# Kernel tuning notes

Measured on AMD Instinct MI355X. Metric: run time of the kernel, lower is better.

The kernel has to match this reference:

```python
import jax, jax.numpy as jnp
import numpy as np

N_HEAD = 16
D_HEAD = 64
D_HIDN = 1024
B, S = 2, 2048
MASK_FILL = -1e9


def setup_inputs() -> dict:
    key = jax.random.key(0)
    ks = jax.random.split(key, 8)
    scale = 1.0 / np.sqrt(D_HIDN)
    return {
        "Q": jax.random.normal(ks[0], (B, S, D_HIDN), dtype=jnp.float32),
        "K": jax.random.normal(ks[1], (B, S, D_HIDN), dtype=jnp.float32),
        "V": jax.random.normal(ks[2], (B, S, D_HIDN), dtype=jnp.float32),
        "attn_mask": jnp.zeros((B, S, S), dtype=jnp.bool_),
        "Wq": jax.random.normal(ks[3], (D_HIDN, N_HEAD * D_HEAD), dtype=jnp.float32) * scale,
        "bq": jnp.zeros((N_HEAD * D_HEAD,), dtype=jnp.float32),
        "Wk": jax.random.normal(ks[4], (D_HIDN, N_HEAD * D_HEAD), dtype=jnp.float32) * scale,
        "bk": jnp.zeros((N_HEAD * D_HEAD,), dtype=jnp.float32),
        "Wv": jax.random.normal(ks[5], (D_HIDN, N_HEAD * D_HEAD), dtype=jnp.float32) * scale,
        "bv": jnp.zeros((N_HEAD * D_HEAD,), dtype=jnp.float32),
        "Wo": jax.random.normal(ks[6], (N_HEAD * D_HEAD, D_HIDN), dtype=jnp.float32) * scale,
        "bo": jnp.zeros((D_HIDN,), dtype=jnp.float32),
    }


def reference(Q, K, V, attn_mask, Wq, bq, Wk, bk, Wv, bv, Wo, bo):
    b, s, _ = Q.shape
    # projections -> [B, H, S, d_head]
    def split_heads(x):
        return x.reshape(b, -1, N_HEAD, D_HEAD).transpose(0, 2, 1, 3)
    q = split_heads(Q @ Wq + bq)
    k = split_heads(K @ Wk + bk)
    v = split_heads(V @ Wv + bv)
    # scaled dot-product attention with masked_fill(-1e9)
    scores = jnp.einsum("bhqd,bhkd->bhqk", q, k) / jnp.sqrt(jnp.float32(D_HEAD))
    scores = jnp.where(attn_mask[:, None, :, :], MASK_FILL, scores)
    attn_prob = jax.nn.softmax(scores, axis=-1)  # [B,H,S,S]
    context = jnp.einsum("bhqk,bhkd->bhqd", attn_prob, v)
    context = context.transpose(0, 2, 1, 3).reshape(b, s, N_HEAD * D_HEAD)
    output = context @ Wo + bo  # dropout is identity at eval
    return output, attn_prob
```

## Files before the change

kernel.cpp:

```cpp
#include <hip/hip_runtime.h>

typedef _Float16 f16;
typedef _Float16 f16x8 __attribute__((ext_vector_type(8)));
typedef float f32x4 __attribute__((ext_vector_type(4)));

#define B_   2
#define S_   2048
#define H_   16
#define DH   64
#define DM   1024
#define BS_  (B_ * S_)

#if __has_builtin(__builtin_amdgcn_exp2f)
#define EXP2(x) __builtin_amdgcn_exp2f(x)
#else
#define EXP2(x) exp2f(x)
#endif

#define SCHED_FENCE() __builtin_amdgcn_sched_barrier(0)

__device__ __forceinline__ void gload16(const void* g, void* l) {
  __builtin_amdgcn_global_load_lds((const __attribute__((address_space(1))) unsigned int*)g,
                                   (__attribute__((address_space(3))) unsigned int*)l, 16, 0, 0);
}

__global__ __launch_bounds__(256) void cvt3(const float* __restrict__ a,
                                            const float* __restrict__ b,
                                            const float* __restrict__ c,
                                            f16* __restrict__ oa,
                                            f16* __restrict__ ob,
                                            f16* __restrict__ oc) {
  int t = blockIdx.y;
  const float* in = t == 0 ? a : (t == 1 ? b : c);
  f16* out = t == 0 ? oa : (t == 1 ? ob : oc);
  int i = (blockIdx.x * 256 + threadIdx.x) * 8;
  float4 x = *(const float4*)(in + i);
  float4 y = *(const float4*)(in + i + 4);
  f16x8 o;
  o[0] = (f16)x.x; o[1] = (f16)x.y; o[2] = (f16)x.z; o[3] = (f16)x.w;
  o[4] = (f16)y.x; o[5] = (f16)y.y; o[6] = (f16)y.z; o[7] = (f16)y.w;
  *(f16x8*)(out + i) = o;
}

__global__ __launch_bounds__(256) void wtrans4(const float* __restrict__ w0, const float* __restrict__ w1,
                                               const float* __restrict__ w2, const float* __restrict__ w3,
                                               f16* __restrict__ t0, f16* __restrict__ t1,
                                               f16* __restrict__ t2, f16* __restrict__ t3) {
  __shared__ float t[64][65];
  int z = blockIdx.z;
  const float* w = z == 0 ? w0 : (z == 1 ? w1 : (z == 2 ? w2 : w3));
  f16* wt = z == 0 ? t0 : (z == 1 ? t1 : (z == 2 ? t2 : t3));
  int r0 = blockIdx.y * 64, c0 = blockIdx.x * 64;
  int tid = threadIdx.x;
  int tr = tid >> 2, seg = tid & 3;
#pragma unroll
  for (int jj = 0; jj < 4; ++jj) {
    float4 v = *(const float4*)(w + (size_t)(r0 + tr) * DM + c0 + seg * 16 + jj * 4);
    t[tr][seg * 16 + jj * 4 + 0] = v.x;
    t[tr][seg * 16 + jj * 4 + 1] = v.y;
    t[tr][seg * 16 + jj * 4 + 2] = v.z;
    t[tr][seg * 16 + jj * 4 + 3] = v.w;
  }
  __syncthreads();
#pragma unroll
  for (int jj = 0; jj < 2; ++jj) {
    f16x8 o;
#pragma unroll
    for (int e = 0; e < 8; ++e) o[e] = (f16)t[seg * 16 + jj * 8 + e][tr];
    *(f16x8*)(wt + (size_t)(c0 + tr) * DM + r0 + seg * 16 + jj * 8) = o;
  }
}

__global__ __launch_bounds__(256) void vtrans(const f16* __restrict__ v,
                                              f16* __restrict__ vt) {
  __shared__ __attribute__((aligned(16))) f16 t[64][72];
  int bh = blockIdx.y;
  int s0 = blockIdx.x * 64;
  const f16* vb = v + (size_t)bh * S_ * DH;
  f16* vtb = vt + (size_t)bh * DH * S_;
  int tid = threadIdx.x;
  int tr = tid >> 2, seg = tid & 3;
  *(f16x8*)&t[tr][seg * 16]     = *(const f16x8*)(vb + (size_t)(s0 + tr) * DH + seg * 16);
  *(f16x8*)&t[tr][seg * 16 + 8] = *(const f16x8*)(vb + (size_t)(s0 + tr) * DH + seg * 16 + 8);
  __syncthreads();
#pragma unroll
  for (int jj = 0; jj < 2; ++jj) {
    f16x8 o;
#pragma unroll
    for (int e = 0; e < 8; ++e) o[e] = t[seg * 16 + jj * 8 + e][tr];
    *(f16x8*)(vtb + (size_t)tr * S_ + s0 + seg * 16 + jj * 8) = o;
  }
}

template <int MODE>
__device__ __forceinline__ void gemm_body(const f16* __restrict__ A,
                                          const f16* __restrict__ Bt,
                                          const float* __restrict__ bias,
                                          f16* __restrict__ outh,
                                          float* __restrict__ outf,
                                          int m0, int n0,
                                          char (&As)[2][16384], char (&Bs)[2][8192]) {
  const int tid = threadIdx.x;
  const int lane = tid & 63, wid = tid >> 6;
  const int wr = wid >> 1, wc = wid & 1;
  const int l15 = lane & 15, l4 = lane >> 4;
  f32x4 acc[4][2];
#pragma unroll
  for (int mi = 0; mi < 4; ++mi)
#pragma unroll
    for (int ni = 0; ni < 2; ++ni) { acc[mi][ni][0]=0.f; acc[mi][ni][1]=0.f; acc[mi][ni][2]=0.f; acc[mi][ni][3]=0.f; }

  auto stage = [&](int buf, int kt) {
#pragma unroll
    for (int j = 0; j < 4; ++j) {
      int L = j * 256 + tid;
      int row = L >> 3, seg = L & 7;
      int so = (seg ^ (row & 7)) << 4;
      gload16((const char*)A + ((size_t)(m0 + row) * DM + kt) * 2 + so,
              As[buf] + j * 4096 + wid * 1024);
    }
#pragma unroll
    for (int j = 0; j < 2; ++j) {
      int L = j * 256 + tid;
      int row = L >> 3, seg = L & 7;
      int so = (seg ^ (row & 7)) << 4;
      gload16((const char*)Bt + ((size_t)(n0 + row) * DM + kt) * 2 + so,
              Bs[buf] + j * 4096 + wid * 1024);
    }
  };

  stage(0, 0);
  __syncthreads();
  for (int t = 0; t < 16; ++t) {
    int cur = t & 1;
    if (t < 15) stage(cur ^ 1, (t + 1) * 64);
#pragma unroll
    for (int kk = 0; kk < 2; ++kk) {
      f16x8 af[4], bf[2];
#pragma unroll
      for (int mi = 0; mi < 4; ++mi) {
        int row = wr * 64 + mi * 16 + l15;
        af[mi] = *(const f16x8*)(As[cur] + row * 128 + ((kk * 64 + l4 * 16) ^ ((row & 7) << 4)));
      }
#pragma unroll
      for (int ni = 0; ni < 2; ++ni) {
        int row = wc * 32 + ni * 16 + l15;
        bf[ni] = *(const f16x8*)(Bs[cur] + row * 128 + ((kk * 64 + l4 * 16) ^ ((row & 7) << 4)));
      }
#pragma unroll
      for (int mi = 0; mi < 4; ++mi)
#pragma unroll
        for (int ni = 0; ni < 2; ++ni)
          acc[mi][ni] = __builtin_amdgcn_mfma_f32_16x16x32_f16(af[mi], bf[ni], acc[mi][ni], 0, 0, 0);
    }
    __syncthreads();
  }
#pragma unroll
  for (int mi = 0; mi < 4; ++mi)
#pragma unroll
    for (int ni = 0; ni < 2; ++ni) {
      int gcol = n0 + wc * 32 + ni * 16 + l15;
      float bv = bias[gcol];
#pragma unroll
      for (int r = 0; r < 4; ++r) {
        int grow = m0 + wr * 64 + mi * 16 + l4 * 4 + r;
        float val = acc[mi][ni][r] + bv;
        if (MODE == 0) {
          int b = grow >> 11, s = grow & 2047, h = gcol >> 6, d = gcol & 63;
          outh[(size_t)((b * H_ + h) * S_ + s) * DH + d] = (f16)val;
        } else {
          outf[(size_t)grow * DM + gcol] = val;
        }
      }
    }
}

struct GemmPtrs { const f16* A; const f16* Bt; const float* bias; f16* outh; };

__global__ __launch_bounds__(256, 3) void gemm_proj(GemmPtrs p0, GemmPtrs p1, GemmPtrs p2) {
  __shared__ __attribute__((aligned(16))) char As[2][16384];
  __shared__ __attribute__((aligned(16))) char Bs[2][8192];
  int lin = (blockIdx.z * 16 + blockIdx.y) * 32 + blockIdx.x;
  int swz = (lin & 7) * 192 + (lin >> 3);
  int z = swz >> 9, r = swz & 511;
  int m0 = (r & 31) * 128, n0 = (r >> 5) * 64;
  GemmPtrs g = z == 0 ? p0 : (z == 1 ? p1 : p2);
  gemm_body<0>(g.A, g.Bt, g.bias, g.outh, nullptr, m0, n0, As, Bs);
}

__global__ __launch_bounds__(256, 3) void gemm_out(const f16* __restrict__ A,
                                                   const f16* __restrict__ Bt,
                                                   const float* __restrict__ bias,
                                                   float* __restrict__ outf) {
  __shared__ __attribute__((aligned(16))) char As[2][16384];
  __shared__ __attribute__((aligned(16))) char Bs[2][8192];
  int lin = blockIdx.y * 32 + blockIdx.x;
  int swz = (lin & 7) * 64 + (lin >> 3);
  int m0 = (swz & 31) * 128, n0 = (swz >> 5) * 64;
  gemm_body<1>(A, Bt, bias, nullptr, outf, m0, n0, As, Bs);
}

__global__ __launch_bounds__(512, 4) void attn_kernel(const f16* __restrict__ q,
                                                      const f16* __restrict__ k,
                                                      const f16* __restrict__ vt,
                                                      const unsigned char* __restrict__ mask,
                                                      float* __restrict__ pout,
                                                      f16* __restrict__ ctxh) {
  __shared__ __attribute__((aligned(16))) char KV[4][8192];
  __shared__ __attribute__((aligned(16))) float P32[8][16][68];
  const int tid = threadIdx.x;
  const int lane = tid & 63, wid = tid >> 6;
  const int l15 = lane & 15, l4 = lane >> 4;

  int lin = blockIdx.y * 16 + blockIdx.x;
  int swz = (lin & 7) * 64 + (lin >> 3);
  const int bx = swz & 15, bh = swz >> 4;
  const int b = bh >> 4, h = bh & 15;
  const int q0w = bx * 128 + wid * 16;

  const f16* qb = q + (size_t)bh * S_ * DH;
  const char* kbc = (const char*)(k + (size_t)bh * S_ * DH);
  const char* vtbc = (const char*)(vt + (size_t)bh * DH * S_);
  const unsigned char* mb = mask + (size_t)b * S_ * S_;
  float* pb = pout + (size_t)bh * S_ * S_;

  const int srow = tid >> 3, sseg = tid & 7;
  const int soff = (sseg ^ (srow & 7)) << 4;

  auto stageK = [&](int buf, int t) {
    gload16(kbc + (size_t)(t * 64 + srow) * 128 + soff, KV[buf] + wid * 1024);
  };
  auto stageV = [&](int buf, int t) {
    gload16(vtbc + (size_t)srow * (S_ * 2) + (size_t)(t * 64) * 2 + soff, KV[buf] + wid * 1024);
  };

  unsigned mmask = 0;
  {
    const unsigned char* mrow = mb + (size_t)(q0w + (lane >> 2)) * S_ + (lane & 3) * 16;
    for (int t = 0; t < 32; ++t) {
      uint4 mu = *(const uint4*)(mrow + t * 64);
      if (__any((mu.x | mu.y | mu.z | mu.w) != 0)) mmask |= 1u << t;
    }
  }

  const f16 qs = (f16)0.18033688f;
  f16x8 aq[2];
#pragma unroll
  for (int hh = 0; hh < 2; ++hh) {
    f16x8 v = *(const f16x8*)(qb + (size_t)(q0w + l15) * DH + hh * 32 + l4 * 8);
#pragma unroll
    for (int j = 0; j < 8; ++j) v[j] = v[j] * qs;
    aq[hh] = v;
  }
  SCHED_FENCE();

  float sm[4] = {0.f, 0.f, 0.f, 0.f};

  stageK(0, 0);
  stageK(1, 1);
  for (int t = 0; t < 32; ++t) {
    if (t < 30) stageK((t + 2) & 3, t + 2);
    SCHED_FENCE();
    if (t < 30)       asm volatile("s_waitcnt vmcnt(2)" ::: "memory");
    else if (t == 30) asm volatile("s_waitcnt vmcnt(1)" ::: "memory");
    else              asm volatile("s_waitcnt vmcnt(0)" ::: "memory");
    __builtin_amdgcn_s_barrier();
    SCHED_FENCE();

    const char* Kb = KV[t & 3];
    const int kt = t * 64;
    const int anym = (mmask >> t) & 1;
#pragma unroll
    for (int f = 0; f < 4; ++f) {
      int krow = f * 16 + l15;
      f16x8 bk0 = *(const f16x8*)(Kb + krow * 128 + ((l4 * 16) ^ ((krow & 7) << 4)));
      f16x8 bk1 = *(const f16x8*)(Kb + krow * 128 + ((64 + l4 * 16) ^ ((krow & 7) << 4)));
      f32x4 s; s[0]=0.f; s[1]=0.f; s[2]=0.f; s[3]=0.f;
      __builtin_amdgcn_s_setprio(1);
      s = __builtin_amdgcn_mfma_f32_16x16x32_f16(aq[0], bk0, s, 0, 0, 0);
      s = __builtin_amdgcn_mfma_f32_16x16x32_f16(aq[1], bk1, s, 0, 0, 0);
      __builtin_amdgcn_s_setprio(0);
#pragma unroll
      for (int r = 0; r < 4; ++r) {
        float sv = s[r];
        if (anym) sv = mb[(size_t)(q0w + l4 * 4 + r) * S_ + kt + f * 16 + l15] ? -1e9f : sv;
        sm[r] += EXP2(sv);
      }
    }
  }
#pragma unroll
  for (int d = 1; d < 16; d <<= 1)
#pragma unroll
    for (int r = 0; r < 4; ++r) sm[r] += __shfl_xor(sm[r], d);
  float inv[4];
#pragma unroll
  for (int r = 0; r < 4; ++r) inv[r] = 1.0f / sm[r];

  f32x4 ctx[4];
#pragma unroll
  for (int dc = 0; dc < 4; ++dc) { ctx[dc][0]=0.f; ctx[dc][1]=0.f; ctx[dc][2]=0.f; ctx[dc][3]=0.f; }

  stageK(0, 0);
  stageV(2, 0);
  __syncthreads();
  for (int t = 0; t < 32; ++t) {
    const int cur = t & 1;
    const int kt = t * 64;
    if (t < 31) { stageK(cur ^ 1, t + 1); stageV(2 + (cur ^ 1), t + 1); }
    SCHED_FENCE();
    const int anym = (mmask >> t) & 1;

#pragma unroll
    for (int f = 0; f < 4; ++f) {
      int krow = f * 16 + l15;
      f16x8 bk0 = *(const f16x8*)(KV[cur] + krow * 128 + ((l4 * 16) ^ ((krow & 7) << 4)));
      f16x8 bk1 = *(const f16x8*)(KV[cur] + krow * 128 + ((64 + l4 * 16) ^ ((krow & 7) << 4)));
      f32x4 s; s[0]=0.f; s[1]=0.f; s[2]=0.f; s[3]=0.f;
      __builtin_amdgcn_s_setprio(1);
      s = __builtin_amdgcn_mfma_f32_16x16x32_f16(aq[0], bk0, s, 0, 0, 0);
      s = __builtin_amdgcn_mfma_f32_16x16x32_f16(aq[1], bk1, s, 0, 0, 0);
      __builtin_amdgcn_s_setprio(0);
#pragma unroll
      for (int r = 0; r < 4; ++r) {
        float sv = s[r];
        if (anym) sv = mb[(size_t)(q0w + l4 * 4 + r) * S_ + kt + f * 16 + l15] ? -1e9f : sv;
        float p = EXP2(sv) * inv[r];
        P32[wid][l4 * 4 + r][f * 16 + l15] = p;
      }
    }
#pragma unroll
    for (int j = 0; j < 4; ++j) {
      int row = j * 4 + l4;
      f32x4 v = *(const f32x4*)&P32[wid][row][l15 * 4];
      __builtin_nontemporal_store(v, (f32x4*)(pb + (size_t)(q0w + row) * S_ + kt + l15 * 4));
    }
#pragma unroll
    for (int kk = 0; kk < 2; ++kk) {
      f32x4 x = *(const f32x4*)&P32[wid][l15][kk * 32 + l4 * 8];
      f32x4 y = *(const f32x4*)&P32[wid][l15][kk * 32 + l4 * 8 + 4];
      f16x8 pa;
      pa[0] = (f16)x[0]; pa[1] = (f16)x[1]; pa[2] = (f16)x[2]; pa[3] = (f16)x[3];
      pa[4] = (f16)y[0]; pa[5] = (f16)y[1]; pa[6] = (f16)y[2]; pa[7] = (f16)y[3];
      f16x8 bv0, bv1, bv2, bv3;
      {
        int vr0 = 0 * 16 + l15, vr1 = 1 * 16 + l15, vr2 = 2 * 16 + l15, vr3 = 3 * 16 + l15;
        bv0 = *(const f16x8*)(KV[2 + cur] + vr0 * 128 + ((kk * 64 + l4 * 16) ^ ((vr0 & 7) << 4)));
        bv1 = *(const f16x8*)(KV[2 + cur] + vr1 * 128 + ((kk * 64 + l4 * 16) ^ ((vr1 & 7) << 4)));
        bv2 = *(const f16x8*)(KV[2 + cur] + vr2 * 128 + ((kk * 64 + l4 * 16) ^ ((vr2 & 7) << 4)));
        bv3 = *(const f16x8*)(KV[2 + cur] + vr3 * 128 + ((kk * 64 + l4 * 16) ^ ((vr3 & 7) << 4)));
      }
      __builtin_amdgcn_s_setprio(1);
      ctx[0] = __builtin_amdgcn_mfma_f32_16x16x32_f16(pa, bv0, ctx[0], 0, 0, 0);
      ctx[1] = __builtin_amdgcn_mfma_f32_16x16x32_f16(pa, bv1, ctx[1], 0, 0, 0);
      ctx[2] = __builtin_amdgcn_mfma_f32_16x16x32_f16(pa, bv2, ctx[2], 0, 0, 0);
      ctx[3] = __builtin_amdgcn_mfma_f32_16x16x32_f16(pa, bv3, ctx[3], 0, 0, 0);
      __builtin_amdgcn_s_setprio(0);
    }

    if (t < 31) {
      asm volatile("s_waitcnt vmcnt(4)" ::: "memory");
      __builtin_amdgcn_s_barrier();
      SCHED_FENCE();
    }
  }

#pragma unroll
  for (int dc = 0; dc < 4; ++dc)
#pragma unroll
    for (int r = 0; r < 4; ++r)
      ctxh[(size_t)(b * S_ + q0w + l4 * 4 + r) * DM + h * DH + dc * 16 + l15] = (f16)ctx[dc][r];
}

extern "C" void kernel_launch(void* const* d_in, const int* in_sizes, int n_in,
                              void* d_out, int out_size, void* d_ws, size_t ws_size,
                              hipStream_t stream) {
  (void)in_sizes; (void)n_in; (void)out_size; (void)ws_size;
  const float* Q  = (const float*)d_in[0];
  const float* K  = (const float*)d_in[1];
  const float* V  = (const float*)d_in[2];
  const unsigned char* mask = (const unsigned char*)d_in[3];
  const float* Wq = (const float*)d_in[4];
  const float* bq = (const float*)d_in[5];
  const float* Wk = (const float*)d_in[6];
  const float* bk = (const float*)d_in[7];
  const float* Wv = (const float*)d_in[8];
  const float* bv = (const float*)d_in[9];
  const float* Wo = (const float*)d_in[10];
  const float* bo = (const float*)d_in[11];

  f16* ws = (f16*)d_ws;
  f16* Xq  = ws;
  f16* Xk  = Xq + 4194304;
  f16* Xv  = Xk + 4194304;
  f16* Wqt = Xv + 4194304;
  f16* Wkt = Wqt + 1048576;
  f16* Wvt = Wkt + 1048576;
  f16* Wot = Wvt + 1048576;
  f16* qh  = Wot + 1048576;
  f16* kh  = qh + 4194304;
  f16* vh  = kh + 4194304;
  f16* vth = Xk;
  f16* ctx = Xq;

  float* out0 = (float*)d_out;
  float* pout = out0 + (size_t)BS_ * DM;

  cvt3<<<dim3(2048, 3), dim3(256), 0, stream>>>(Q, K, V, Xq, Xk, Xv);
  wtrans4<<<dim3(16, 16, 4), dim3(256), 0, stream>>>(Wq, Wk, Wv, Wo, Wqt, Wkt, Wvt, Wot);

  GemmPtrs pq{Xq, Wqt, bq, qh};
  GemmPtrs pk{Xk, Wkt, bk, kh};
  GemmPtrs pv{Xv, Wvt, bv, vh};
  gemm_proj<<<dim3(32, 16, 3), dim3(256), 0, stream>>>(pq, pk, pv);

  vtrans<<<dim3(32, 32), dim3(256), 0, stream>>>(vh, vth);

  attn_kernel<<<dim3(16, 32), dim3(512), 0, stream>>>(qh, kh, vth, mask, pout, ctx);

  gemm_out<<<dim3(32, 16), dim3(256), 0, stream>>>(ctx, Wot, bo, out0);
}
```

Before: 238.7 us.

## Fuse V transpose into projection GEMM, batch mask scan, unroll softmax-sum pass

The V projection now writes its output already transposed, staged through shared memory inside the projection GEMM epilogue, so the separate vtrans kernel and its round trip through memory are gone. The GEMM tile mapping is changed so consecutive blocks walk along N instead of M. The attention kernel's mask prescan first ORs all mask bytes with batched loads and only falls back to the per-tile scan when something is set. The first softmax pass now processes two K tiles per barrier with a full vmcnt(0) wait. The added LDS staging and the coarser wait in the sum pass could reduce overlap.

```diff
diff --git a/kernel.cpp b/kernel.cpp
--- a/kernel.cpp
+++ b/kernel.cpp
@@ -2,6 +2,7 @@
 
 typedef _Float16 f16;
 typedef _Float16 f16x8 __attribute__((ext_vector_type(8)));
+typedef _Float16 f16x4v __attribute__((ext_vector_type(4)));
 typedef float f32x4 __attribute__((ext_vector_type(4)));
 
 #define B_   2
@@ -71,40 +72,15 @@
   }
 }
 
-__global__ __launch_bounds__(256) void vtrans(const f16* __restrict__ v,
-                                              f16* __restrict__ vt) {
-  __shared__ __attribute__((aligned(16))) f16 t[64][72];
-  int bh = blockIdx.y;
-  int s0 = blockIdx.x * 64;
-  const f16* vb = v + (size_t)bh * S_ * DH;
-  f16* vtb = vt + (size_t)bh * DH * S_;
-  int tid = threadIdx.x;
-  int tr = tid >> 2, seg = tid & 3;
-  *(f16x8*)&t[tr][seg * 16]     = *(const f16x8*)(vb + (size_t)(s0 + tr) * DH + seg * 16);
-  *(f16x8*)&t[tr][seg * 16 + 8] = *(const f16x8*)(vb + (size_t)(s0 + tr) * DH + seg * 16 + 8);
-  __syncthreads();
-#pragma unroll
-  for (int jj = 0; jj < 2; ++jj) {
-    f16x8 o;
-#pragma unroll
-    for (int e = 0; e < 8; ++e) o[e] = t[seg * 16 + jj * 8 + e][tr];
-    *(f16x8*)(vtb + (size_t)tr * S_ + s0 + seg * 16 + jj * 8) = o;
-  }
-}
-
-template <int MODE>
-__device__ __forceinline__ void gemm_body(const f16* __restrict__ A,
+__device__ __forceinline__ void gemm_core(const f16* __restrict__ A,
                                           const f16* __restrict__ Bt,
-                                          const float* __restrict__ bias,
-                                          f16* __restrict__ outh,
-                                          float* __restrict__ outf,
                                           int m0, int n0,
-                                          char (&As)[2][16384], char (&Bs)[2][8192]) {
+                                          char (&As)[2][16384], char (&Bs)[2][8192],
+                                          f32x4 (&acc)[4][2]) {
   const int tid = threadIdx.x;
   const int lane = tid & 63, wid = tid >> 6;
   const int wr = wid >> 1, wc = wid & 1;
   const int l15 = lane & 15, l4 = lane >> 4;
-  f32x4 acc[4][2];
 #pragma unroll
   for (int mi = 0; mi < 4; ++mi)
 #pragma unroll
@@ -155,37 +131,67 @@
     }
     __syncthreads();
   }
-#pragma unroll
-  for (int mi = 0; mi < 4; ++mi)
-#pragma unroll
-    for (int ni = 0; ni < 2; ++ni) {
-      int gcol = n0 + wc * 32 + ni * 16 + l15;
-      float bv = bias[gcol];
-#pragma unroll
-      for (int r = 0; r < 4; ++r) {
-        int grow = m0 + wr * 64 + mi * 16 + l4 * 4 + r;
-        float val = acc[mi][ni][r] + bv;
-        if (MODE == 0) {
-          int b = grow >> 11, s = grow & 2047, h = gcol >> 6, d = gcol & 63;
-          outh[(size_t)((b * H_ + h) * S_ + s) * DH + d] = (f16)val;
-        } else {
-          outf[(size_t)grow * DM + gcol] = val;
-        }
-      }
-    }
 }
 
 struct GemmPtrs { const f16* A; const f16* Bt; const float* bias; f16* outh; };
 
-__global__ __launch_bounds__(256, 3) void gemm_proj(GemmPtrs p0, GemmPtrs p1, GemmPtrs p2) {
+__global__ __launch_bounds__(256, 3) void gemm_proj(GemmPtrs p0, GemmPtrs p1, GemmPtrs p2,
+                                                    f16* __restrict__ vout) {
   __shared__ __attribute__((aligned(16))) char As[2][16384];
   __shared__ __attribute__((aligned(16))) char Bs[2][8192];
   int lin = (blockIdx.z * 16 + blockIdx.y) * 32 + blockIdx.x;
   int swz = (lin & 7) * 192 + (lin >> 3);
   int z = swz >> 9, r = swz & 511;
-  int m0 = (r & 31) * 128, n0 = (r >> 5) * 64;
+  int m0 = (r >> 4) * 128, n0 = (r & 15) * 64;
   GemmPtrs g = z == 0 ? p0 : (z == 1 ? p1 : p2);
-  gemm_body<0>(g.A, g.Bt, g.bias, g.outh, nullptr, m0, n0, As, Bs);
+
+  f32x4 acc[4][2];
+  gemm_core(g.A, g.Bt, m0, n0, As, Bs, acc);
+
+  const int tid = threadIdx.x;
+  const int lane = tid & 63, wid = tid >> 6;
+  const int wr = wid >> 1, wc = wid & 1;
+  const int l15 = lane & 15, l4 = lane >> 4;
+
+  if (z != 2) {
+#pragma unroll
+    for (int mi = 0; mi < 4; ++mi)
+#pragma unroll
+      for (int ni = 0; ni < 2; ++ni) {
+        int gcol = n0 + wc * 32 + ni * 16 + l15;
+        float bv = g.bias[gcol];
+#pragma unroll
+        for (int rr = 0; rr < 4; ++rr) {
+          int grow = m0 + wr * 64 + mi * 16 + l4 * 4 + rr;
+          int b = grow >> 11, s = grow & 2047, h = gcol >> 6, d = gcol & 63;
+          g.outh[(size_t)((b * H_ + h) * S_ + s) * DH + d] = (f16)(acc[mi][ni][rr] + bv);
+        }
+      }
+  } else {
+    f16* T2 = (f16*)&As[0][0];
+#pragma unroll
+    for (int mi = 0; mi < 4; ++mi)
+#pragma unroll
+      for (int ni = 0; ni < 2; ++ni) {
+        int d = wc * 32 + ni * 16 + l15;
+        int sl = wr * 64 + mi * 16 + l4 * 4;
+        float bv = g.bias[n0 + d];
+        f16x4v pv;
+        pv[0] = (f16)(acc[mi][ni][0] + bv);
+        pv[1] = (f16)(acc[mi][ni][1] + bv);
+        pv[2] = (f16)(acc[mi][ni][2] + bv);
+        pv[3] = (f16)(acc[mi][ni][3] + bv);
+        *(f16x4v*)(T2 + d * 136 + sl) = pv;
+      }
+    __syncthreads();
+    int d = tid >> 2, sq = tid & 3;
+    int b = m0 >> 11, s0 = m0 & 2047, h = n0 >> 6;
+    const f16* src = T2 + d * 136 + sq * 32;
+    f16* dst = vout + ((size_t)((b * H_ + h) * DH + d)) * S_ + s0 + sq * 32;
+#pragma unroll
+    for (int j = 0; j < 4; ++j)
+      *(f16x8*)(dst + j * 8) = *(const f16x8*)(src + j * 8);
+  }
 }
 
 __global__ __launch_bounds__(256, 3) void gemm_out(const f16* __restrict__ A,
@@ -196,8 +202,27 @@
   __shared__ __attribute__((aligned(16))) char Bs[2][8192];
   int lin = blockIdx.y * 32 + blockIdx.x;
   int swz = (lin & 7) * 64 + (lin >> 3);
-  int m0 = (swz & 31) * 128, n0 = (swz >> 5) * 64;
-  gemm_body<1>(A, Bt, bias, nullptr, outf, m0, n0, As, Bs);
+  int m0 = (swz >> 4) * 128, n0 = (swz & 15) * 64;
+
+  f32x4 acc[4][2];
+  gemm_core(A, Bt, m0, n0, As, Bs, acc);
+
+  const int tid = threadIdx.x;
+  const int lane = tid & 63, wid = tid >> 6;
+  const int wr = wid >> 1, wc = wid & 1;
+  const int l15 = lane & 15, l4 = lane >> 4;
+#pragma unroll
+  for (int mi = 0; mi < 4; ++mi)
+#pragma unroll
+    for (int ni = 0; ni < 2; ++ni) {
+      int gcol = n0 + wc * 32 + ni * 16 + l15;
+      float bv = bias[gcol];
+#pragma unroll
+      for (int rr = 0; rr < 4; ++rr) {
+        int grow = m0 + wr * 64 + mi * 16 + l4 * 4 + rr;
+        outf[(size_t)grow * DM + gcol] = acc[mi][ni][rr] + bv;
+      }
+    }
 }
 
 __global__ __launch_bounds__(512, 4) void attn_kernel(const f16* __restrict__ q,
@@ -237,9 +262,20 @@
   unsigned mmask = 0;
   {
     const unsigned char* mrow = mb + (size_t)(q0w + (lane >> 2)) * S_ + (lane & 3) * 16;
-    for (int t = 0; t < 32; ++t) {
-      uint4 mu = *(const uint4*)(mrow + t * 64);
-      if (__any((mu.x | mu.y | mu.z | mu.w) != 0)) mmask |= 1u << t;
+    unsigned acc_or = 0;
+#pragma unroll
+    for (int tt = 0; tt < 4; ++tt) {
+      uint4 mu[8];
+#pragma unroll
+      for (int u = 0; u < 8; ++u) mu[u] = *(const uint4*)(mrow + (tt * 8 + u) * 64);
+#pragma unroll
+      for (int u = 0; u < 8; ++u) acc_or |= mu[u].x | mu[u].y | mu[u].z | mu[u].w;
+    }
+    if (__any(acc_or != 0)) {
+      for (int t = 0; t < 32; ++t) {
+        uint4 mu = *(const uint4*)(mrow + t * 64);
+        if (__any((mu.x | mu.y | mu.z | mu.w) != 0)) mmask |= 1u << t;
+      }
     }
   }
 
@@ -258,48 +294,50 @@
 
   stageK(0, 0);
   stageK(1, 1);
-  for (int t = 0; t < 32; ++t) {
-    if (t < 30) stageK((t + 2) & 3, t + 2);
-    SCHED_FENCE();
-    if (t < 30)       asm volatile("s_waitcnt vmcnt(2)" ::: "memory");
-    else if (t == 30) asm volatile("s_waitcnt vmcnt(1)" ::: "memory");
-    else              asm volatile("s_waitcnt vmcnt(0)" ::: "memory");
+  for (int p = 0; p < 16; ++p) {
+    asm volatile("s_waitcnt vmcnt(0)" ::: "memory");
     __builtin_amdgcn_s_barrier();
     SCHED_FENCE();
-
-    const char* Kb = KV[t & 3];
-    const int kt = t * 64;
-    const int anym = (mmask >> t) & 1;
-#pragma unroll
-    for (int f = 0; f < 4; ++f) {
-      int krow = f * 16 + l15;
-      f16x8 bk0 = *(const f16x8*)(Kb + krow * 128 + ((l4 * 16) ^ ((krow & 7) << 4)));
-      f16x8 bk1 = *(const f16x8*)(Kb + krow * 128 + ((64 + l4 * 16) ^ ((krow & 7) << 4)));
-      f32x4 s; s[0]=0.f; s[1]=0.f; s[2]=0.f; s[3]=0.f;
-      __builtin_amdgcn_s_setprio(1);
-      s = __builtin_amdgcn_mfma_f32_16x16x32_f16(aq[0], bk0, s, 0, 0, 0);
-      s = __builtin_amdgcn_mfma_f32_16x16x32_f16(aq[1], bk1, s, 0, 0, 0);
-      __builtin_amdgcn_s_setprio(0);
-#pragma unroll
-      for (int r = 0; r < 4; ++r) {
-        float sv = s[r];
-        if (anym) sv = mb[(size_t)(q0w + l4 * 4 + r) * S_ + kt + f * 16 + l15] ? -1e9f : sv;
-        sm[r] += EXP2(sv);
+    if (p < 15) { stageK((2 * p + 2) & 3, 2 * p + 2); stageK((2 * p + 3) & 3, 2 * p + 3); }
+    SCHED_FENCE();
+#pragma unroll
+    for (int u = 0; u < 2; ++u) {
+      const int t = 2 * p + u;
+      const char* Kb = KV[t & 3];
+      const int kt = t * 64;
+      const int anym = (mmask >> t) & 1;
+#pragma unroll
+      for (int f = 0; f < 4; ++f) {
+        int krow = f * 16 + l15;
+        f16x8 bk0 = *(const f16x8*)(Kb + krow * 128 + ((l4 * 16) ^ ((krow & 7) << 4)));
+        f16x8 bk1 = *(const f16x8*)(Kb + krow * 128 + ((64 + l4 * 16) ^ ((krow & 7) << 4)));
+        f32x4 s; s[0]=0.f; s[1]=0.f; s[2]=0.f; s[3]=0.f;
+        __builtin_amdgcn_s_setprio(1);
+        s = __builtin_amdgcn_mfma_f32_16x16x32_f16(aq[0], bk0, s, 0, 0, 0);
+        s = __builtin_amdgcn_mfma_f32_16x16x32_f16(aq[1], bk1, s, 0, 0, 0);
+        __builtin_amdgcn_s_setprio(0);
+#pragma unroll
+        for (int rr = 0; rr < 4; ++rr) {
+          float sv = s[rr];
+          if (anym) sv = mb[(size_t)(q0w + l4 * 4 + rr) * S_ + kt + f * 16 + l15] ? -1e9f : sv;
+          sm[rr] += EXP2(sv);
+        }
       }
     }
   }
 #pragma unroll
   for (int d = 1; d < 16; d <<= 1)
 #pragma unroll
-    for (int r = 0; r < 4; ++r) sm[r] += __shfl_xor(sm[r], d);
+    for (int rr = 0; rr < 4; ++rr) sm[rr] += __shfl_xor(sm[rr], d);
   float inv[4];
 #pragma unroll
-  for (int r = 0; r < 4; ++r) inv[r] = 1.0f / sm[r];
+  for (int rr = 0; rr < 4; ++rr) inv[rr] = 1.0f / sm[rr];
 
   f32x4 ctx[4];
 #pragma unroll
   for (int dc = 0; dc < 4; ++dc) { ctx[dc][0]=0.f; ctx[dc][1]=0.f; ctx[dc][2]=0.f; ctx[dc][3]=0.f; }
 
+  __builtin_amdgcn_s_barrier();
   stageK(0, 0);
   stageV(2, 0);
   __syncthreads();
@@ -321,11 +359,11 @@
       s = __builtin_amdgcn_mfma_f32_16x16x32_f16(aq[1], bk1, s, 0, 0, 0);
       __builtin_amdgcn_s_setprio(0);
 #pragma unroll
-      for (int r = 0; r < 4; ++r) {
-        float sv = s[r];
-        if (anym) sv = mb[(size_t)(q0w + l4 * 4 + r) * S_ + kt + f * 16 + l15] ? -1e9f : sv;
-        float p = EXP2(sv) * inv[r];
-        P32[wid][l4 * 4 + r][f * 16 + l15] = p;
+      for (int rr = 0; rr < 4; ++rr) {
+        float sv = s[rr];
+        if (anym) sv = mb[(size_t)(q0w + l4 * 4 + rr) * S_ + kt + f * 16 + l15] ? -1e9f : sv;
+        float p = EXP2(sv) * inv[rr];
+        P32[wid][l4 * 4 + rr][f * 16 + l15] = p;
       }
     }
 #pragma unroll
@@ -367,8 +405,8 @@
 #pragma unroll
   for (int dc = 0; dc < 4; ++dc)
 #pragma unroll
-    for (int r = 0; r < 4; ++r)
-      ctxh[(size_t)(b * S_ + q0w + l4 * 4 + r) * DM + h * DH + dc * 16 + l15] = (f16)ctx[dc][r];
+    for (int rr = 0; rr < 4; ++rr)
+      ctxh[(size_t)(b * S_ + q0w + l4 * 4 + rr) * DM + h * DH + dc * 16 + l15] = (f16)ctx[dc][rr];
 }
 
 extern "C" void kernel_launch(void* const* d_in, const int* in_sizes, int n_in,
@@ -398,8 +436,7 @@
   f16* Wot = Wvt + 1048576;
   f16* qh  = Wot + 1048576;
   f16* kh  = qh + 4194304;
-  f16* vh  = kh + 4194304;
-  f16* vth = Xk;
+  f16* vth = kh + 4194304;
   f16* ctx = Xq;
 
   float* out0 = (float*)d_out;
@@ -410,10 +447,8 @@
 
   GemmPtrs pq{Xq, Wqt, bq, qh};
   GemmPtrs pk{Xk, Wkt, bk, kh};
-  GemmPtrs pv{Xv, Wvt, bv, vh};
-  gemm_proj<<<dim3(32, 16, 3), dim3(256), 0, stream>>>(pq, pk, pv);
-
-  vtrans<<<dim3(32, 32), dim3(256), 0, stream>>>(vh, vth);
+  GemmPtrs pv{Xv, Wvt, bv, nullptr};
+  gemm_proj<<<dim3(32, 16, 3), dim3(256), 0, stream>>>(pq, pk, pv, vth);
 
   attn_kernel<<<dim3(16, 32), dim3(512), 0, stream>>>(qh, kh, vth, mask, pout, ctx);
 
```

New measurement: 229.7 us. -3.7%, faster.
